# Optimization experiments

Measured on AMD Instinct MI355X. Metric: run time of the kernel, lower is better.

The kernel has to match this reference:

```python
import jax, jax.numpy as jnp
import numpy as np


def setup_inputs() -> dict:
    key = jax.random.key(0)
    k1, k2, k3 = jax.random.split(key, 3)
    B, H, L, D = 4, 16, 1024, 64
    q = jax.random.normal(k1, (B, H, L, D), dtype=jnp.float32)
    k = jax.random.normal(k2, (B, H, L, D), dtype=jnp.float32)
    attn_mask = jax.random.randint(k3, (B, H, L, L), 0, 2).astype(bool)
    return {"q": q, "k": k, "attn_mask": attn_mask}


def reference(q, k, attn_mask):
    # q, k: [B, H, L, D]. The original builds a [B,H,L,D,L] tensor
    # c[b,h,i,m,j] = exp(-(q[b,h,i,m]-k[b,h,j,m])^2), then for each dim m
    # keeps only the entries where rank of q[i,m] (along seq) equals rank of
    # k[j,m], scatters them into an LxL grid and averages over m.
    # Equivalent fused form: sort q and k per dimension, pair equal ranks,
    # and scatter-add exp(-(q_sorted - k_sorted)^2)/D into p[b,h,i,j].
    B, H, L, D = q.shape
    q_idx = jnp.argsort(q, axis=2)                       # [B,H,L,D] int
    k_idx = jnp.argsort(k, axis=2)
    q_sorted = jnp.take_along_axis(q, q_idx, axis=2)     # [B,H,L,D]
    k_sorted = jnp.take_along_axis(k, k_idx, axis=2)
    diff = q_sorted - k_sorted
    vals = jnp.exp(-(diff * diff))                       # [B,H,L,D]
    # linear index into the flattened [L,L] grid, plus batch*head offset
    lin = q_idx * L + k_idx                              # [B,H,L,D]
    bh_off = (jnp.arange(B * H) * (L * L)).reshape(B, H, 1, 1)
    flat_idx = (lin + bh_off).ravel()
    p = jnp.zeros(B * H * L * L, dtype=q.dtype).at[flat_idx].add(vals.ravel())
    p = (p / D).reshape(B, H, L, L)
    return jnp.where(attn_mask, jnp.zeros((), dtype=p.dtype), p)
```

## Files before the change

### kernel.cpp

```cpp
#include <hip/hip_runtime.h>
#include <stdint.h>
#include <string.h>


#define LL 1024
#define DD 64
#define NBH 64
#define MAT_WORDS ((size_t)NBH * DD * LL)
#define WS_BYTES (3 * MAT_WORDS * 4)

typedef float    vf4   __attribute__((ext_vector_type(4)));
typedef uint32_t vu4   __attribute__((ext_vector_type(4)));
typedef int32_t  vi4   __attribute__((ext_vector_type(4)));

__device__ __forceinline__ uint32_t f2ord(float x) {
    uint32_t u = __float_as_uint(x);
    return (u & 0x80000000u) ? ~u : (u | 0x80000000u);
}
__device__ __forceinline__ float ord2f(uint32_t o) {
    uint32_t u = (o & 0x80000000u) ? (o & 0x7fffffffu) : ~o;
    return __uint_as_float(u);
}
__device__ __forceinline__ void cex(uint64_t& a, uint64_t& b, bool up) {
    const uint64_t lo = a < b ? a : b;
    const uint64_t hi = a < b ? b : a;
    a = up ? lo : hi; b = up ? hi : lo;
}
__device__ __forceinline__ uint64_t shfl64(uint64_t v, int m) {
    const uint32_t lo = __shfl_xor((uint32_t)v, m);
    const uint32_t hi = __shfl_xor((uint32_t)(v >> 32), m);
    return ((uint64_t)hi << 32) | lo;
}

__device__ __forceinline__ void wave_bitonic16(uint64_t x[16], const int lane) {
    #pragma unroll
    for (int lk = 1; lk <= 3; ++lk) {
        const int k2 = 1 << lk;
        #pragma unroll
        for (int j = k2 >> 1; j >= 1; j >>= 1) {
            #pragma unroll
            for (int s = 0; s < 16; ++s)
                if ((s & j) == 0) cex(x[s], x[s | j], ((s & k2) == 0));
        }
    }
    {
        const bool up = ((lane & 1) == 0);
        #pragma unroll
        for (int j = 8; j >= 1; j >>= 1) {
            #pragma unroll
            for (int s = 0; s < 16; ++s)
                if ((s & j) == 0) cex(x[s], x[s | j], up);
        }
    }
    #pragma unroll
    for (int lk = 5; lk <= 10; ++lk) {
        const bool up = ((lane & (1 << (lk - 4))) == 0);
        #pragma unroll
        for (int m = 1 << (lk - 5); m >= 1; m >>= 1) {
            const bool keepmin = (((lane & m) == 0) == up);
            #pragma unroll
            for (int s = 0; s < 16; ++s) {
                const uint64_t y = shfl64(x[s], m);
                x[s] = keepmin ? (x[s] < y ? x[s] : y)
                               : (x[s] > y ? x[s] : y);
            }
        }
        #pragma unroll
        for (int j = 8; j >= 1; j >>= 1) {
            #pragma unroll
            for (int s = 0; s < 16; ++s)
                if ((s & j) == 0) cex(x[s], x[s | j], up);
        }
    }
}

__global__ __launch_bounds__(256) void swd3_transpose(
    const float* __restrict__ q, const float* __restrict__ k,
    uint32_t* __restrict__ qt, uint32_t* __restrict__ kt)
{
    __shared__ uint32_t tq[64][65];
    __shared__ uint32_t tk[64][65];

    const int b  = blockIdx.x;
    const int bh = (b & 7) * 8 + ((b >> 3) & 7);
    const int e0 = (b >> 6) * 64;
    const int t  = threadIdx.x;

    const size_t base = (size_t)bh * (LL * DD);
    #pragma unroll
    for (int i = 0; i < 4; ++i) {
        const int idx = i * 256 + t;
        const int r   = idx >> 4;
        const int c   = (idx & 15) * 4;
        const vf4 vq = *(const vf4*)(q + base + (size_t)(e0 + r) * DD + c);
        const vf4 vk = *(const vf4*)(k + base + (size_t)(e0 + r) * DD + c);
        tq[r][c + 0] = f2ord(vq.x); tq[r][c + 1] = f2ord(vq.y);
        tq[r][c + 2] = f2ord(vq.z); tq[r][c + 3] = f2ord(vq.w);
        tk[r][c + 0] = f2ord(vk.x); tk[r][c + 1] = f2ord(vk.y);
        tk[r][c + 2] = f2ord(vk.z); tk[r][c + 3] = f2ord(vk.w);
    }
    __syncthreads();
    #pragma unroll
    for (int i = 0; i < 4; ++i) {
        const int idx = i * 256 + t;
        const int d   = idx >> 4;
        const int c   = (idx & 15) * 4;
        vu4 v;
        v.x = tq[c + 0][d]; v.y = tq[c + 1][d];
        v.z = tq[c + 2][d]; v.w = tq[c + 3][d];
        *(vu4*)(qt + base + (size_t)d * LL + e0 + c) = v;
        v.x = tk[c + 0][d]; v.y = tk[c + 1][d];
        v.z = tk[c + 2][d]; v.w = tk[c + 3][d];
        *(vu4*)(kt + base + (size_t)d * LL + e0 + c) = v;
    }
}

__global__ __launch_bounds__(256, 3) void swd3_phase1(
    const uint32_t* __restrict__ qt, const uint32_t* __restrict__ kt,
    uint32_t* __restrict__ pairs)
{
    __shared__ alignas(16) uint32_t pr[4][LL];

    const int raw  = blockIdx.x;
    const int slot = raw >> 3;
    const int bh   = (raw & 7) * 8 + (slot >> 4);
    const int dg   = slot & 15;
    const int t    = threadIdx.x;
    const int w    = t >> 6;
    const int lane = t & 63;
    const int d    = dg * 4 + w;

    const uint32_t* colq = qt + (size_t)bh * (DD * LL) + (size_t)d * LL;
    const uint32_t* colk = kt + (size_t)bh * (DD * LL) + (size_t)d * LL;

    uint64_t xq[16], xk[16];
    #pragma unroll
    for (int r = 0; r < 4; ++r) {
        const vu4 vq = *(const vu4*)(colq + 256 * r + 4 * lane);
        const vu4 vk = *(const vu4*)(colk + 256 * r + 4 * lane);
        const uint32_t eb = 256u * r + 4u * lane;
        xq[4 * r + 0] = ((uint64_t)vq.x << 32) | (eb + 0);
        xq[4 * r + 1] = ((uint64_t)vq.y << 32) | (eb + 1);
        xq[4 * r + 2] = ((uint64_t)vq.z << 32) | (eb + 2);
        xq[4 * r + 3] = ((uint64_t)vq.w << 32) | (eb + 3);
        xk[4 * r + 0] = ((uint64_t)vk.x << 32) | (eb + 0);
        xk[4 * r + 1] = ((uint64_t)vk.y << 32) | (eb + 1);
        xk[4 * r + 2] = ((uint64_t)vk.z << 32) | (eb + 2);
        xk[4 * r + 3] = ((uint64_t)vk.w << 32) | (eb + 3);
    }
    wave_bitonic16(xq, lane);
    wave_bitonic16(xk, lane);

    uint32_t* prw = pr[w];
    #pragma unroll
    for (int s = 0; s < 16; ++s) {
        const uint32_t iq = (uint32_t)xq[s] & 1023u;
        const uint32_t ik = (uint32_t)xk[s] & 1023u;
        const float df = ord2f((uint32_t)(xq[s] >> 32))
                       - ord2f((uint32_t)(xk[s] >> 32));
        const float val = __expf(-df * df) * (1.0f / 64.0f);
        prw[iq] = (__float_as_uint(val) & 0xFFFFFC00u) | ik;
    }
    __asm__ volatile("s_waitcnt lgkmcnt(0)" ::: "memory");
    vu4* pp4 = (vu4*)(pairs + ((size_t)bh * DD + d) * LL);
    const vu4* src = (const vu4*)prw;
    #pragma unroll
    for (int r = 0; r < 4; ++r)
        pp4[r * 64 + lane] = src[r * 64 + lane];
}

__global__ __launch_bounds__(256) void swd3_phase2(
    const uint32_t* __restrict__ pairs, const void* __restrict__ maskp,
    float* __restrict__ out)
{
    __shared__ alignas(16) float acc[8 * LL];
    __shared__ uint32_t sdet[4];

    const int b  = blockIdx.x;
    const int bh = (b & 7) * 8 + ((b >> 3) & 7);
    const int st = b >> 6;
    const int i0 = st * 8;
    const int t  = threadIdx.x;

    {
        const uint32_t w = ((const uint32_t*)maskp)[t];
        const uint64_t bal = __ballot(w > 1u);
        if ((t & 63) == 0) sdet[t >> 6] = (bal != 0ull) ? 1u : 0u;
    }

    vf4* acc4 = (vf4*)acc;
    #pragma unroll
    for (int v = 0; v < 8; ++v) {
        vf4 z; z.x = 0.f; z.y = 0.f; z.z = 0.f; z.w = 0.f;
        acc4[v * 256 + t] = z;
    }
    __syncthreads();

    const bool mask_byte =
        ((sdet[0] | sdet[1] | sdet[2] | sdet[3]) != 0u);
    const size_t cellbase = ((size_t)bh << 20) + ((size_t)i0 << 10);

    uint32_t mb[8];
    vi4      mi[8];
    if (mask_byte) {
        const uint32_t* mp = (const uint32_t*)maskp + (cellbase >> 2);
        #pragma unroll
        for (int v = 0; v < 8; ++v)
            mb[v] = __builtin_nontemporal_load(mp + v * 256 + t);
    } else {
        const vi4* mp = (const vi4*)((const int32_t*)maskp + cellbase);
        #pragma unroll
        for (int v = 0; v < 8; ++v)
            mi[v] = __builtin_nontemporal_load(mp + v * 256 + t);
    }

    {
        const uint32_t* pb = pairs + (size_t)bh * (DD * LL);
        const int dd = t >> 2;
        const uint2 pv = ((const uint2*)(pb + dd * LL + i0))[t & 3];
        const int ii0 = 2 * (t & 3), ii1 = ii0 + 1;
        atomicAdd(&acc[ii0 * LL + (int)(pv.x & 1023u)],
                  __uint_as_float(pv.x & 0xFFFFFC00u));
        atomicAdd(&acc[ii1 * LL + (int)(pv.y & 1023u)],
                  __uint_as_float(pv.y & 0xFFFFFC00u));
    }
    __syncthreads();

    vf4* ob = (vf4*)(out + cellbase);
    #pragma unroll
    for (int v = 0; v < 8; ++v) {
        const int p = v * 256 + t;
        const vf4 a = acc4[p];
        int mx, my, mz, mw2;
        if (mask_byte) {
            const uint32_t m = mb[v];
            mx = (int)(m & 0xFFu); my = (int)((m >> 8) & 0xFFu);
            mz = (int)((m >> 16) & 0xFFu); mw2 = (int)(m >> 24);
        } else {
            mx = mi[v].x; my = mi[v].y; mz = mi[v].z; mw2 = mi[v].w;
        }
        vf4 r;
        r.x = mx  ? 0.f : a.x;
        r.y = my  ? 0.f : a.y;
        r.z = mz  ? 0.f : a.z;
        r.w = mw2 ? 0.f : a.w;
        __builtin_nontemporal_store(r, ob + p);
    }
}

extern "C" void kernel_launch(void* const* d_in, const int* in_sizes, int n_in,
                              void* d_out, int out_size, void* d_ws, size_t ws_size,
                              hipStream_t stream) {
    const float* q = (const float*)d_in[0];
    const float* k = (const float*)d_in[1];
    const void* mask = d_in[2];
    uint32_t* pairs = (uint32_t*)d_ws;
    uint32_t* qt = pairs + MAT_WORDS;
    uint32_t* kt = qt + MAT_WORDS;

    const bool ws_ok = (ws_size >= WS_BYTES);
    hipError_t e0 = hipSuccess, e1 = hipSuccess, e2 = hipSuccess;
    (void)hipGetLastError();

    if (ws_ok) {
        swd3_transpose<<<NBH * 16, 256, 0, stream>>>(q, k, qt, kt);
        e0 = hipGetLastError();
        swd3_phase1<<<NBH * DD / 4, 256, 0, stream>>>(qt, kt, pairs);
        e1 = hipGetLastError();
        swd3_phase2<<<NBH * 128, 256, 0, stream>>>(pairs, mask, (float*)d_out);
        e2 = hipGetLastError();
    }

    if (!ws_ok || e0 != hipSuccess || e1 != hipSuccess || e2 != hipSuccess) {
        static float h_stamp[8];
        h_stamp[0] = !ws_ok ? (9000.0f + (float)(ws_size >> 20))
                            : (1000.0f + (float)(int)e0);
        h_stamp[1] = 2000.0f + (float)(int)e1;
        h_stamp[2] = 3000.0f + (float)(int)e2;
        h_stamp[3] = h_stamp[0];
        hipMemcpyAsync(d_out, h_stamp, sizeof(h_stamp),
                       hipMemcpyHostToDevice, stream);
    }
}
```

Before: 551.8 us.

## Replace shuffle bitonic sort with mirror-merge sort using DPP and swizzle

Rewrites the per-wave 1024-element sort into a merge network where every stage sorts in one direction, using mirror (reversal) exchanges in place of direction-dependent bitonic steps. Cross-lane exchanges move from __shfl_xor (ds_bpermute through LDS hardware) to DPP row ops for small distances, ds_swizzle for 16/31, and bpermute only for the 63-mirror step. This is meant to cut the LDS-routed permute cost and the per-element direction selects in phase1. It adds more complex lane-pattern code whose correctness depends on the DPP control encodings.

New measurement: 508.0 us (median of 2 runs). -7.9%, faster.

```diff
diff --git a/kernel.cpp b/kernel.cpp
--- a/kernel.cpp
+++ b/kernel.cpp
@@ -21,57 +21,134 @@
     uint32_t u = (o & 0x80000000u) ? (o & 0x7fffffffu) : ~o;
     return __uint_as_float(u);
 }
-__device__ __forceinline__ void cex(uint64_t& a, uint64_t& b, bool up) {
-    const uint64_t lo = a < b ? a : b;
-    const uint64_t hi = a < b ? b : a;
-    a = up ? lo : hi; b = up ? hi : lo;
-}
-__device__ __forceinline__ uint64_t shfl64(uint64_t v, int m) {
-    const uint32_t lo = __shfl_xor((uint32_t)v, m);
-    const uint32_t hi = __shfl_xor((uint32_t)(v >> 32), m);
+
+template <int CTRL>
+__device__ __forceinline__ uint64_t dpp64(uint64_t v) {
+    const uint32_t lo = (uint32_t)__builtin_amdgcn_update_dpp(
+        0, (int)(uint32_t)v, CTRL, 0xF, 0xF, true);
+    const uint32_t hi = (uint32_t)__builtin_amdgcn_update_dpp(
+        0, (int)(uint32_t)(v >> 32), CTRL, 0xF, 0xF, true);
     return ((uint64_t)hi << 32) | lo;
 }
-
-__device__ __forceinline__ void wave_bitonic16(uint64_t x[16], const int lane) {
-    #pragma unroll
-    for (int lk = 1; lk <= 3; ++lk) {
-        const int k2 = 1 << lk;
+template <int PATT>
+__device__ __forceinline__ uint64_t swz64(uint64_t v) {
+    const uint32_t lo = (uint32_t)__builtin_amdgcn_ds_swizzle(
+        (int)(uint32_t)v, PATT);
+    const uint32_t hi = (uint32_t)__builtin_amdgcn_ds_swizzle(
+        (int)(uint32_t)(v >> 32), PATT);
+    return ((uint64_t)hi << 32) | lo;
+}
+__device__ __forceinline__ uint64_t bper64(uint64_t v, int addr) {
+    const uint32_t lo = (uint32_t)__builtin_amdgcn_ds_bpermute(
+        addr, (int)(uint32_t)v);
+    const uint32_t hi = (uint32_t)__builtin_amdgcn_ds_bpermute(
+        addr, (int)(uint32_t)(v >> 32));
+    return ((uint64_t)hi << 32) | lo;
+}
+__device__ __forceinline__ uint64_t fx1 (uint64_t v){ return dpp64<0xB1>(v); }
+__device__ __forceinline__ uint64_t fx2 (uint64_t v){ return dpp64<0x4E>(v); }
+__device__ __forceinline__ uint64_t fx3 (uint64_t v){ return dpp64<0x1B>(v); }
+__device__ __forceinline__ uint64_t fx4 (uint64_t v){ return dpp64<0x1B>(dpp64<0x141>(v)); }
+__device__ __forceinline__ uint64_t fx7 (uint64_t v){ return dpp64<0x141>(v); }
+__device__ __forceinline__ uint64_t fx8 (uint64_t v){ return dpp64<0x141>(dpp64<0x140>(v)); }
+__device__ __forceinline__ uint64_t fx15(uint64_t v){ return dpp64<0x140>(v); }
+__device__ __forceinline__ uint64_t fx16(uint64_t v){ return swz64<0x401F>(v); }
+__device__ __forceinline__ uint64_t fx31(uint64_t v){ return swz64<0x7C1F>(v); }
+
+__device__ __forceinline__ void wave_sort1024(uint64_t x[16], const int lane,
+                                              const int addr63)
+{
+    auto cexA = [](uint64_t& a, uint64_t& b) {
+        const uint64_t lo = a < b ? a : b;
+        const uint64_t hi = a < b ? b : a;
+        a = lo; b = hi;
+    };
+    auto sel = [](uint64_t xv, uint64_t y, bool km) {
+        return ((xv < y) == km) ? xv : y;
+    };
+
+#define TAIL4() do { _Pragma("unroll") \
+    for (int j = 8; j >= 1; j >>= 1) { _Pragma("unroll") \
+        for (int s = 0; s < 16; ++s) \
+            if (!(s & j)) cexA(x[s], x[s | j]); } } while (0)
+
+#define MIRROR(F, KM) do { _Pragma("unroll") \
+    for (int i = 0; i < 8; ++i) { \
+        const uint64_t ya = F(x[15 - i]); \
+        const uint64_t yb = F(x[i]); \
+        x[i]      = sel(x[i],      ya, (KM)); \
+        x[15 - i] = sel(x[15 - i], yb, (KM)); } } while (0)
+
+#define XORST(F, KM) do { _Pragma("unroll") \
+    for (int s = 0; s < 16; ++s) { \
+        const uint64_t y = F(x[s]); \
+        x[s] = sel(x[s], y, (KM)); } } while (0)
+
+    #pragma unroll
+    for (int s = 0; s < 16; s += 2) cexA(x[s], x[s + 1]);
+    #pragma unroll
+    for (int b = 0; b < 16; b += 4) {
+        cexA(x[b], x[b + 3]); cexA(x[b + 1], x[b + 2]);
+    }
+    #pragma unroll
+    for (int s = 0; s < 16; s += 2) cexA(x[s], x[s + 1]);
+    #pragma unroll
+    for (int b = 0; b < 16; b += 8) {
+        cexA(x[b], x[b + 7]); cexA(x[b + 1], x[b + 6]);
+        cexA(x[b + 2], x[b + 5]); cexA(x[b + 3], x[b + 4]);
+    }
+    #pragma unroll
+    for (int j = 2; j >= 1; j >>= 1) {
         #pragma unroll
-        for (int j = k2 >> 1; j >= 1; j >>= 1) {
-            #pragma unroll
-            for (int s = 0; s < 16; ++s)
-                if ((s & j) == 0) cex(x[s], x[s | j], ((s & k2) == 0));
-        }
-    }
-    {
-        const bool up = ((lane & 1) == 0);
+        for (int s = 0; s < 16; ++s)
+            if (!(s & j)) cexA(x[s], x[s | j]);
+    }
+    #pragma unroll
+    for (int i = 0; i < 8; ++i) cexA(x[i], x[15 - i]);
+    #pragma unroll
+    for (int j = 4; j >= 1; j >>= 1) {
         #pragma unroll
-        for (int j = 8; j >= 1; j >>= 1) {
-            #pragma unroll
-            for (int s = 0; s < 16; ++s)
-                if ((s & j) == 0) cex(x[s], x[s | j], up);
-        }
-    }
-    #pragma unroll
-    for (int lk = 5; lk <= 10; ++lk) {
-        const bool up = ((lane & (1 << (lk - 4))) == 0);
-        #pragma unroll
-        for (int m = 1 << (lk - 5); m >= 1; m >>= 1) {
-            const bool keepmin = (((lane & m) == 0) == up);
-            #pragma unroll
-            for (int s = 0; s < 16; ++s) {
-                const uint64_t y = shfl64(x[s], m);
-                x[s] = keepmin ? (x[s] < y ? x[s] : y)
-                               : (x[s] > y ? x[s] : y);
-            }
-        }
-        #pragma unroll
-        for (int j = 8; j >= 1; j >>= 1) {
-            #pragma unroll
-            for (int s = 0; s < 16; ++s)
-                if ((s & j) == 0) cex(x[s], x[s | j], up);
-        }
-    }
+        for (int s = 0; s < 16; ++s)
+            if (!(s & j)) cexA(x[s], x[s | j]);
+    }
+
+    { const bool km = (lane & 1) == 0;
+      MIRROR(fx1, km); TAIL4(); }
+    { const bool kmM = (lane & 2) == 0;
+      MIRROR(fx3, kmM);
+      const bool k1 = (lane & 1) == 0; XORST(fx1, k1); TAIL4(); }
+    { const bool kmM = (lane & 4) == 0;
+      MIRROR(fx7, kmM);
+      const bool k2 = (lane & 2) == 0; XORST(fx2, k2);
+      const bool k1 = (lane & 1) == 0; XORST(fx1, k1); TAIL4(); }
+    { const bool kmM = (lane & 8) == 0;
+      MIRROR(fx15, kmM);
+      const bool k4 = (lane & 4) == 0; XORST(fx4, k4);
+      const bool k2 = (lane & 2) == 0; XORST(fx2, k2);
+      const bool k1 = (lane & 1) == 0; XORST(fx1, k1); TAIL4(); }
+    { const bool kmM = (lane & 16) == 0;
+      MIRROR(fx31, kmM);
+      const bool k8 = (lane & 8) == 0; XORST(fx8, k8);
+      const bool k4 = (lane & 4) == 0; XORST(fx4, k4);
+      const bool k2 = (lane & 2) == 0; XORST(fx2, k2);
+      const bool k1 = (lane & 1) == 0; XORST(fx1, k1); TAIL4(); }
+    { const bool kmM = (lane & 32) == 0;
+      #pragma unroll
+      for (int i = 0; i < 8; ++i) {
+          const uint64_t ya = bper64(x[15 - i], addr63);
+          const uint64_t yb = bper64(x[i], addr63);
+          x[i]      = sel(x[i],      ya, kmM);
+          x[15 - i] = sel(x[15 - i], yb, kmM);
+      }
+      const bool k16 = (lane & 16) == 0; XORST(fx16, k16);
+      const bool k8  = (lane & 8)  == 0; XORST(fx8,  k8);
+      const bool k4  = (lane & 4)  == 0; XORST(fx4,  k4);
+      const bool k2  = (lane & 2)  == 0; XORST(fx2,  k2);
+      const bool k1  = (lane & 1)  == 0; XORST(fx1,  k1); TAIL4(); }
+
+#undef TAIL4
+#undef MIRROR
+#undef XORST
 }
 
 __global__ __launch_bounds__(256) void swd3_transpose(
@@ -129,6 +206,7 @@
     const int w    = t >> 6;
     const int lane = t & 63;
     const int d    = dg * 4 + w;
+    const int addr63 = (lane ^ 63) << 2;
 
     const uint32_t* colq = qt + (size_t)bh * (DD * LL) + (size_t)d * LL;
     const uint32_t* colk = kt + (size_t)bh * (DD * LL) + (size_t)d * LL;
@@ -148,8 +226,8 @@
         xk[4 * r + 2] = ((uint64_t)vk.z << 32) | (eb + 2);
         xk[4 * r + 3] = ((uint64_t)vk.w << 32) | (eb + 3);
     }
-    wave_bitonic16(xq, lane);
-    wave_bitonic16(xk, lane);
+    wave_sort1024(xq, lane, addr63);
+    wave_sort1024(xk, lane, addr63);
 
     uint32_t* prw = pr[w];
     #pragma unroll
```
